# Optimization experiments

Measured on AMD Instinct MI355X. Metric: run time of the kernel, lower is better.

The kernel has to match this reference:

```python
import jax, jax.numpy as jnp
import numpy as np


def _conv3x3(x, w, b):
    # standard 3x3 conv, stride 1, padding 1, NCHW/OIHW
    y = jax.lax.conv_general_dilated(
        x, w, window_strides=(1, 1), padding=((1, 1), (1, 1)),
        dimension_numbers=('NCHW', 'OIHW', 'NCHW'))
    return y + b[None, :, None, None]


def _deform_conv3x3(x, offset, w, b):
    # torchvision-style DeformConv2d: kernel 3x3, stride 1, pad 1, dilation 1,
    # 1 offset group, no mask. offset: [B, 18, H, W] with (dy, dx) per tap.
    B, C, H, W = x.shape
    K = 9
    off = offset.reshape(B, K, 2, H, W)
    ky = (jnp.arange(K) // 3 - 1).astype(x.dtype)[None, :, None, None]
    kx = (jnp.arange(K) % 3 - 1).astype(x.dtype)[None, :, None, None]
    # fractional sample positions per output pixel and kernel tap: [B, K, H, W]
    sy = off[:, :, 0] + ky + jnp.arange(H, dtype=x.dtype)[None, None, :, None]
    sx = off[:, :, 1] + kx + jnp.arange(W, dtype=x.dtype)[None, None, None, :]
    y0f = jnp.floor(sy)
    x0f = jnp.floor(sx)
    dy = sy - y0f
    dx = sx - x0f
    y0 = y0f.astype(jnp.int32)
    x0 = x0f.astype(jnp.int32)

    def sample_b(xb, yi, xi):
        # xb: [C,H,W], yi/xi: [K,H,W] -> [C,K,H,W], zero outside bounds
        valid = (yi >= 0) & (yi < H) & (xi >= 0) & (xi < W)
        yc = jnp.clip(yi, 0, H - 1)
        xc = jnp.clip(xi, 0, W - 1)
        return xb[:, yc, xc] * valid[None].astype(xb.dtype)

    def bilinear_b(xb, y0b, x0b, dyb, dxb):
        v00 = sample_b(xb, y0b, x0b)
        v01 = sample_b(xb, y0b, x0b + 1)
        v10 = sample_b(xb, y0b + 1, x0b)
        v11 = sample_b(xb, y0b + 1, x0b + 1)
        w00 = ((1 - dyb) * (1 - dxb))[None]
        w01 = ((1 - dyb) * dxb)[None]
        w10 = (dyb * (1 - dxb))[None]
        w11 = (dyb * dxb)[None]
        return v00 * w00 + v01 * w01 + v10 * w10 + v11 * w11

    samp = jax.vmap(bilinear_b)(x, y0, x0, dy, dx)  # [B, C, K, H, W]
    Co, Ci = w.shape[0], w.shape[1]
    out = jnp.einsum('oik,bikhw->bohw', w.reshape(Co, Ci, K), samp)
    return out + b[None, :, None, None]


def setup_inputs() -> dict:
    key = jax.random.key(0)
    ks = jax.random.split(key, 5)
    B, C, H, W = 4, 128, 96, 96
    lr = jax.random.normal(ks[0], (B, C, H, W), jnp.float32)
    hr = jax.random.normal(ks[1], (B, C, H, W), jnp.float32)
    w_off = jax.random.normal(ks[2], (18, 2 * C, 3, 3), jnp.float32) * 0.02
    b_off = jnp.zeros((18,), jnp.float32)
    w_def = jax.random.normal(ks[3], (C, C, 3, 3), jnp.float32) / np.float32(np.sqrt(C * 9))
    b_def = jax.random.normal(ks[4], (C,), jnp.float32) * 0.01
    return {"lr_features": lr, "hr_features": hr, "w_off": w_off,
            "b_off": b_off, "w_def": w_def, "b_def": b_def}


def reference(lr_features, hr_features, w_off, b_off, w_def, b_def):
    inp = jnp.concatenate([lr_features, hr_features], axis=1)  # [B, 2C, H, W]
    offset = _conv3x3(inp, w_off, b_off)                        # [B, 18, H, W]
    return _deform_conv3x3(hr_features, offset, w_def, b_def)   # [B, C, H, W]
```

## Files before the change

### kernel.cpp

```cpp
#include <hip/hip_runtime.h>
#include <hip/hip_bf16.h>

#define HH 96
#define WW 96
#define CC 128
#define C2 256
#define PLANE (HH*WW)
#define NGRP 6
#define GP 8
#define NG 16
#define KSG 72
#define ROWS 13
#define NPCHK (ROWS*WW)
#define PCHK_PAD 1280

typedef __attribute__((ext_vector_type(8))) short bf16x8;
typedef __attribute__((ext_vector_type(4))) float f32x4;
typedef __attribute__((ext_vector_type(4))) unsigned int u32x4;

__device__ __forceinline__ int swz(int row, int byte_in_row) {
    return row * 128 + (byte_in_row ^ ((row & 7) << 4));
}

__device__ __forceinline__ void gload_lds16(const void* g, void* l) {
    __builtin_amdgcn_global_load_lds(
        (const __attribute__((address_space(1))) char*)g,
        (__attribute__((address_space(3))) char*)l, 16, 0, 0);
}

__device__ __forceinline__ unsigned pack2(float a, float b) {
    return (unsigned)__bfloat16_as_ushort(__float2bfloat16(a)) |
           ((unsigned)__bfloat16_as_ushort(__float2bfloat16(b)) << 16);
}

#define MFMA16(A,B,C) __builtin_amdgcn_mfma_f32_16x16x32_bf16((A),(B),(C),0,0,0)

#define VMW4() { asm volatile("s_waitcnt vmcnt(4)" ::: "memory"); __builtin_amdgcn_sched_barrier(0); }
#define VMW0() { asm volatile("s_waitcnt vmcnt(0)" ::: "memory"); __builtin_amdgcn_sched_barrier(0); }
#define LGKM0_BAR() { asm volatile("s_waitcnt lgkmcnt(0)" ::: "memory"); \
    __builtin_amdgcn_sched_barrier(0); __builtin_amdgcn_s_barrier(); \
    __builtin_amdgcn_sched_barrier(0); }
#define RAW_BAR() { __builtin_amdgcn_sched_barrier(0); __builtin_amdgcn_s_barrier(); \
    __builtin_amdgcn_sched_barrier(0); }

__global__ __launch_bounds__(256) void prep_kernel(
    const float* __restrict__ hr, const float* __restrict__ lr,
    const float* __restrict__ w_def, const float* __restrict__ w_off,
    unsigned short* __restrict__ hrbf, unsigned short* __restrict__ lrbf,
    unsigned short* __restrict__ wpad, unsigned short* __restrict__ wop)
{
    const int bid = blockIdx.x;
    const int tid = threadIdx.x;
    if (bid < 4608) {
        const bool is_hr = bid < 2304;
        const float* src0 = is_hr ? hr : lr;
        unsigned short* o = is_hr ? hrbf : lrbf;
        int idx = (is_hr ? bid : bid - 2304) * 256 + tid;
        int hw = idx % PLANE;
        int t  = idx / PLANE;
        int g  = t & 15;
        int b  = t >> 4;
        const float* src = src0 + ((size_t)(b * CC + g * GP)) * PLANE + hw;
        unsigned pk[4];
#pragma unroll
        for (int j = 0; j < 4; ++j)
            pk[j] = pack2(src[(size_t)(2*j) * PLANE], src[(size_t)(2*j+1) * PLANE]);
        u32x4 v = {pk[0], pk[1], pk[2], pk[3]};
        *reinterpret_cast<u32x4*>(o + (size_t)idx * 8) = v;
    } else if (bid < 5184) {
        int i = (bid - 4608) * 256 + tid;
        int oc = i / (NG * KSG);
        int r  = i - oc * (NG * KSG);
        int g  = r / KSG;
        int s  = r - g * KSG;
        int tap = s >> 3;
        int icoff = s & 7;
        wpad[i] = __bfloat16_as_ushort(__float2bfloat16(
            w_def[(size_t)(oc * CC + g * GP + icoff) * 9 + tap]));
    } else {
        int i = (bid - 5184) * 256 + tid;
        int oc = i / (32 * KSG);
        int r  = i - oc * (32 * KSG);
        int g  = r / KSG;
        int s  = r - g * KSG;
        int tap = s >> 3;
        int icoff = s & 7;
        int c = g * 8 + icoff;
        float v = (oc < 18) ? w_off[(size_t)(oc * C2 + c) * 9 + tap] : 0.f;
        wop[i] = __bfloat16_as_ushort(__float2bfloat16(v));
    }
}

__global__ __launch_bounds__(256) void wcvt_kernel(const float* __restrict__ w,
                                                   unsigned short* __restrict__ o)
{
    int i = blockIdx.x * 256 + threadIdx.x;
    if (i < CC * NG * KSG) {
        int oc = i / (NG * KSG);
        int r  = i - oc * (NG * KSG);
        int g  = r / KSG;
        int s  = r - g * KSG;
        int tap = s >> 3;
        int icoff = s & 7;
        o[i] = __bfloat16_as_ushort(__float2bfloat16(
            w[(size_t)(oc * CC + g * GP + icoff) * 9 + tap]));
    }
}

__global__ __launch_bounds__(256) void cvt8_kernel(const float* __restrict__ src0,
                                                   unsigned short* __restrict__ o)
{
    int idx = blockIdx.x * 256 + threadIdx.x;
    int hw = idx % PLANE;
    int t  = idx / PLANE;
    int g  = t & 15;
    int b  = t >> 4;
    const float* src = src0 + ((size_t)(b * CC + g * GP)) * PLANE + hw;
    unsigned pk[4];
#pragma unroll
    for (int j = 0; j < 4; ++j)
        pk[j] = pack2(src[(size_t)(2*j) * PLANE], src[(size_t)(2*j+1) * PLANE]);
    u32x4 v = {pk[0], pk[1], pk[2], pk[3]};
    *reinterpret_cast<u32x4*>(o + (size_t)idx * 8) = v;
}

__global__ __launch_bounds__(256) void offset_conv_kernel(
    const float* __restrict__ lr, const float* __restrict__ hr,
    const float* __restrict__ w_off, float* __restrict__ outp)
{
    __shared__ float tile[2][324];
    const int bid = blockIdx.x;
    const int q   = bid % NGRP;
    const int t   = bid / NGRP;
    const int b   = t / 36;
    const int rr  = t % 36;
    const int h0  = (rr / 6) * 16;
    const int w0  = (rr % 6) * 16;
    const int tid = threadIdx.x;
    const int py  = tid >> 4;
    const int px  = tid & 15;

    const int c0 = (C2 * q) / NGRP, c1 = (C2 * (q + 1)) / NGRP;
    const float* srcp = (q < 3) ? lr : hr;
    const int cofs = (q < 3) ? 0 : CC;

    int gy0 = h0 - 1 + tid / 18, gx0 = w0 - 1 + tid % 18;
    bool ok0 = (unsigned)gy0 < (unsigned)HH && (unsigned)gx0 < (unsigned)WW;
    int off0 = gy0 * WW + gx0;
    int j1 = tid + 256;
    int gy1 = h0 - 1 + j1 / 18, gx1 = w0 - 1 + j1 % 18;
    bool ok1 = (j1 < 324) && (unsigned)gy1 < (unsigned)HH && (unsigned)gx1 < (unsigned)WW;
    int off1 = gy1 * WW + gx1;

    float acc[18];
#pragma unroll
    for (int oc = 0; oc < 18; ++oc) acc[oc] = 0.f;

    const float* pl = srcp + (size_t)(b * CC + c0 - cofs) * PLANE;
    float p0 = ok0 ? pl[off0] : 0.f;
    float p1 = ok1 ? pl[off1] : 0.f;

    for (int c = c0; c < c1; ++c) {
        float* tb = tile[c & 1];
        tb[tid] = p0;
        if (j1 < 324) tb[j1] = p1;
        __syncthreads();
        if (c + 1 < c1) {
            const float* pn = srcp + (size_t)(b * CC + c + 1 - cofs) * PLANE;
            p0 = ok0 ? pn[off0] : 0.f;
            p1 = ok1 ? pn[off1] : 0.f;
        }
        float tv[9];
#pragma unroll
        for (int ky = 0; ky < 3; ++ky)
#pragma unroll
            for (int kx = 0; kx < 3; ++kx)
                tv[ky*3+kx] = tb[(py+ky)*18 + px + kx];
#pragma unroll
        for (int oc = 0; oc < 18; ++oc) {
            const float* wp = w_off + (size_t)(oc * C2 + c) * 9;
#pragma unroll
            for (int tap = 0; tap < 9; ++tap)
                acc[oc] = fmaf(wp[tap], tv[tap], acc[oc]);
        }
    }
#pragma unroll
    for (int oc = 0; oc < 18; ++oc)
        outp[((size_t)(b*CC + q*18 + oc)) * PLANE + (h0+py)*WW + (w0+px)] = acc[oc];
}

__global__ __launch_bounds__(768, 6) void offset_mfma_kernel(
    const unsigned short* __restrict__ lrbf, const unsigned short* __restrict__ hrbf,
    const unsigned short* __restrict__ wop, const float* __restrict__ b_off,
    float* __restrict__ offw)
{
    __shared__ __align__(16) unsigned short planes[2][2][3*WW*8];
    __shared__ __align__(16) unsigned short wgt0[2][32*64];
    __shared__ __align__(16) unsigned short wgt1[2][32*8];
    __shared__ __align__(16) unsigned short samp0[2][WW*64];
    __shared__ __align__(16) unsigned short samp1[2][WW*8];

    const int rawb = blockIdx.x;
    const int bid  = (rawb & 7) * 48 + (rawb >> 3);
    const int b    = bid / HH;
    const int h    = bid % HH;
    const int tid  = threadIdx.x;

    const int pri = tid / 96, ppx = tid - (tid / 96) * 96;
    const int prow = min(max(h - 1 + pri, 0), HH - 1);

    const int woc = tid / 9, wsl = tid % 9;
    float4 wv0, wv1;

#define ISSUE_P2(PAIR, PB) { \
    if (tid < 288) { \
        int gA_ = 2*(PAIR), gB_ = gA_ + 1; \
        const unsigned short* bA_ = (gA_ < 16 ? lrbf : hrbf); \
        const unsigned short* bB_ = (gB_ < 16 ? lrbf : hrbf); \
        gload_lds16(bA_ + ((size_t)(b*16 + (gA_ & 15)) * PLANE + prow*WW + ppx) * 8, \
                    (char*)planes[PB][0] + tid*16); \
        gload_lds16(bB_ + ((size_t)(b*16 + (gB_ & 15)) * PLANE + prow*WW + ppx) * 8, \
                    (char*)planes[PB][1] + tid*16); \
    } }
#define ISSUE_W2(PAIR) { \
    if (tid < 288) { \
        wv0 = *reinterpret_cast<const float4*>(wop + ((size_t)(woc*32 + 2*(PAIR)    ))*KSG + wsl*8); \
        wv1 = *reinterpret_cast<const float4*>(wop + ((size_t)(woc*32 + 2*(PAIR) + 1))*KSG + wsl*8); \
    } }
#define WRITE_W2() { \
    if (tid < 288) { \
        if (wsl < 8) { \
            *reinterpret_cast<float4*>((char*)wgt0[0] + swz(woc, wsl*16)) = wv0; \
            *reinterpret_cast<float4*>((char*)wgt0[1] + swz(woc, wsl*16)) = wv1; \
        } else { \
            *reinterpret_cast<float4*>((char*)wgt1[0] + woc*16) = wv0; \
            *reinterpret_cast<float4*>((char*)wgt1[1] + woc*16) = wv1; \
        } \
    } }

    const int tap1 = tid / WW, px1 = tid - (tid / WW) * WW;
    const int ky1 = tap1 / 3 - 1, kx1 = tap1 % 3 - 1;
    const int row1 = h + ky1, x1 = px1 + kx1;
    const bool ok1 = (unsigned)row1 < (unsigned)HH && (unsigned)x1 < (unsigned)WW;
    const int ro1 = ((ky1+1)*WW + x1) * 16;
    const int wr1 = px1*128 + ((tap1*16) ^ ((px1 & 7) << 4));
    const int x2 = tid + 1;
    const bool ok2 = (tid < 96) && (h + 1 < HH) && (x2 < WW);
    const int ro2 = (2*WW + x2) * 16;
    const int wr2 = tid * 16;

    const int lane = tid & 63;
    const int wid  = tid >> 6;
    const int ocg  = wid / 6;
    const int pxg  = wid - ocg * 6;
    const int l15  = lane & 15;
    const int l4   = lane >> 4;
    const int rowA = ocg*16 + l15;
    const int rowB = pxg*16 + l15;
    const bf16x8 zf = {};

    f32x4 acc = (f32x4){0.f, 0.f, 0.f, 0.f};

#define MFMA_O2() { \
    _Pragma("unroll") \
    for (int q_ = 0; q_ < 2; ++q_) { \
        bf16x8 a0_ = *reinterpret_cast<const bf16x8*>((char*)wgt0[q_] + swz(rowA, l4*16)); \
        bf16x8 a1_ = *reinterpret_cast<const bf16x8*>((char*)wgt0[q_] + swz(rowA, 64 + l4*16)); \
        bf16x8 a2_ = *reinterpret_cast<const bf16x8*>((char*)wgt1[q_] + rowA*16); \
        if (l4) a2_ = zf; \
        bf16x8 b0_ = *reinterpret_cast<const bf16x8*>((char*)samp0[q_] + swz(rowB, l4*16)); \
        bf16x8 b1_ = *reinterpret_cast<const bf16x8*>((char*)samp0[q_] + swz(rowB, 64 + l4*16)); \
        bf16x8 b2_ = *reinterpret_cast<const bf16x8*>((char*)samp1[q_] + rowB*16); \
        acc = MFMA16(a0_, b0_, acc); \
        acc = MFMA16(a1_, b1_, acc); \
        acc = MFMA16(a2_, b2_, acc); \
    } }

    ISSUE_W2(0);
    ISSUE_P2(0, 0);
    __syncthreads();

    for (int p2 = 0; p2 < 16; ++p2) {
        const int sb = p2 & 1;
        WRITE_W2();
        if (p2 < 15) {
            ISSUE_W2(p2 + 1);
            ISSUE_P2(p2 + 1, sb ^ 1);
            VMW4();
        } else {
            VMW0();
        }
        RAW_BAR();
        {
            u32x4 vA = {0u, 0u, 0u, 0u}, vB = {0u, 0u, 0u, 0u};
            if (ok1) {
                vA = *reinterpret_cast<const u32x4*>((const char*)planes[sb][0] + ro1);
                vB = *reinterpret_cast<const u32x4*>((const char*)planes[sb][1] + ro1);
            }
            *reinterpret_cast<u32x4*>((char*)samp0[0] + wr1) = vA;
            *reinterpret_cast<u32x4*>((char*)samp0[1] + wr1) = vB;
            if (tid < 96) {
                u32x4 wA = {0u, 0u, 0u, 0u}, wB = {0u, 0u, 0u, 0u};
                if (ok2) {
                    wA = *reinterpret_cast<const u32x4*>((const char*)planes[sb][0] + ro2);
                    wB = *reinterpret_cast<const u32x4*>((const char*)planes[sb][1] + ro2);
                }
                *reinterpret_cast<u32x4*>((char*)samp1[0] + wr2) = wA;
                *reinterpret_cast<u32x4*>((char*)samp1[1] + wr2) = wB;
            }
        }
        LGKM0_BAR();
        __builtin_amdgcn_s_setprio(1);
        MFMA_O2();
        __builtin_amdgcn_s_setprio(0);
        RAW_BAR();
    }

#pragma unroll
    for (int r = 0; r < 4; ++r) {
        int oc = ocg*16 + l4*4 + r;
        if (oc < 18)
            offw[((size_t)(b*18 + oc)) * PLANE + h*WW + pxg*16 + l15] = acc[r] + b_off[oc];
    }
#undef ISSUE_P2
#undef ISSUE_W2
#undef WRITE_W2
#undef MFMA_O2
}

template<bool HRBF, bool OFFWS>
__global__ __launch_bounds__(768, 6) void deform2_kernel(
    const float* __restrict__ hr, const unsigned short* __restrict__ hrbf,
    const float* __restrict__ b_off, const unsigned short* __restrict__ wpad,
    const float* __restrict__ b_def, const float* __restrict__ offw,
    float* __restrict__ outp)
{
    __shared__ __align__(16) unsigned short planes[2][PCHK_PAD*8];
    __shared__ __align__(16) unsigned short wgt0[CC*64];
    __shared__ __align__(16) unsigned short wgt1[CC*8];
    __shared__ __align__(16) unsigned short samp0[WW*64];
    __shared__ __align__(16) unsigned short samp1[WW*8];
    __shared__ __align__(8)  float2 geom[9*97];
    __shared__ float bias_lds[CC];

    const int rawb = blockIdx.x;
    const int bid  = (rawb & 7) * 48 + (rawb >> 3);
    const int b    = bid / HH;
    const int h    = bid % HH;
    const int tid  = threadIdx.x;
    const int r0   = min(max(h - 6, 0), HH - ROWS);

    const float* hrb = hr + (size_t)b * CC * PLANE;

    float4 wv0, wv1;
    const int wc0oc = tid / 9, wc0s = tid % 9;
    const int wt2   = (tid < 384) ? tid + 768 : tid;
    const int wc1oc = wt2 / 9, wc1s = wt2 % 9;
    const int pc2   = (tid < 512) ? tid + 768 : tid;
    const int pcs   = min(pc2, NPCHK - 1);

#define ISSUE_WGT(G) { \
    wv0 = *reinterpret_cast<const float4*>(wpad + ((size_t)(wc0oc*NG + (G))*KSG + wc0s*8)); \
    wv1 = *reinterpret_cast<const float4*>(wpad + ((size_t)(wc1oc*NG + (G))*KSG + wc1s*8)); }
#define WRITE_WGT() { \
    if (wc0s < 8) *reinterpret_cast<float4*>((char*)wgt0 + swz(wc0oc, wc0s*16)) = wv0; \
    else          *reinterpret_cast<float4*>((char*)wgt1 + wc0oc*16) = wv0; \
    if (tid < 384) { \
        if (wc1s < 8) *reinterpret_cast<float4*>((char*)wgt0 + swz(wc1oc, wc1s*16)) = wv1; \
        else          *reinterpret_cast<float4*>((char*)wgt1 + wc1oc*16) = wv1; \
    } }

#define ISSUE_PLANES(G, PB) { \
    const unsigned short* src_ = hrbf + ((size_t)(b*NG + (G))*PLANE + r0*WW)*8; \
    gload_lds16(src_ + (size_t)tid*8, (char*)planes[PB] + tid*16); \
    gload_lds16(src_ + (size_t)pcs*8, (char*)planes[PB] + pc2*16); }

#define STAGE_DIRECT(G, PB) { \
    for (int p = tid; p < NPCHK; p += 768) { \
        int r_ = p / WW, x_ = p - (p / WW) * WW; \
        const float* s_ = hrb + (size_t)((G)*GP) * PLANE + (r0 + r_)*WW + x_; \
        unsigned pk_[4]; \
        _Pragma("unroll") \
        for (int j = 0; j < 4; ++j) \
            pk_[j] = pack2(s_[(size_t)(2*j)*PLANE], s_[(size_t)(2*j+1)*PLANE]); \
        u32x4 v_ = {pk_[0], pk_[1], pk_[2], pk_[3]}; \
        *reinterpret_cast<u32x4*>((char*)planes[PB] + p*16) = v_; \
    } }

    if (HRBF) ISSUE_PLANES(0, 0);
    ISSUE_WGT(0);

    for (int t = tid; t < 9 * WW; t += 768) {
        int tap = t / WW;
        int px  = t - tap * WW;
        int hw  = h * WW + px;
        float offy, offx;
        if (OFFWS) {
            offy = offw[((size_t)(b*18 + 2*tap    )) * PLANE + hw];
            offx = offw[((size_t)(b*18 + 2*tap + 1)) * PLANE + hw];
        } else {
            offy = b_off[2*tap]; offx = b_off[2*tap + 1];
#pragma unroll
            for (int q = 0; q < NGRP; ++q) {
                offy += outp[((size_t)(b*CC + q*18 + 2*tap    )) * PLANE + hw];
                offx += outp[((size_t)(b*CC + q*18 + 2*tap + 1)) * PLANE + hw];
            }
        }
        geom[tap*97 + px] = make_float2((float)h  + (float)(tap/3 - 1) + offy,
                                        (float)px + (float)(tap%3 - 1) + offx);
    }
    if (tid < CC) bias_lds[tid] = b_def[tid];
    if (!HRBF) STAGE_DIRECT(0, 0);
    __syncthreads();

    const int lane = tid & 63;
    const int wid  = tid >> 6;
    const int ocg4 = wid / 3;
    const int pxg  = wid - ocg4 * 3;
    const int l15  = lane & 15;
    const int l4   = lane >> 4;

    f32x4 acc[2][2];
#pragma unroll
    for (int mf = 0; mf < 2; ++mf)
#pragma unroll
        for (int nf = 0; nf < 2; ++nf)
            acc[mf][nf] = (f32x4){0.f, 0.f, 0.f, 0.f};

    const int rowA0 = ocg4*32 + l15, rowA1 = rowA0 + 16;
    const int rowB0 = pxg*32 + l15,  rowB1 = rowB0 + 16;
    const bf16x8 zf = {};

#define MFMA_G() { \
    bf16x8 a00_ = *reinterpret_cast<const bf16x8*>((char*)wgt0 + swz(rowA0, l4*16)); \
    bf16x8 a10_ = *reinterpret_cast<const bf16x8*>((char*)wgt0 + swz(rowA1, l4*16)); \
    bf16x8 a01_ = *reinterpret_cast<const bf16x8*>((char*)wgt0 + swz(rowA0, 64 + l4*16)); \
    bf16x8 a11_ = *reinterpret_cast<const bf16x8*>((char*)wgt0 + swz(rowA1, 64 + l4*16)); \
    bf16x8 a02_ = *reinterpret_cast<const bf16x8*>((char*)wgt1 + rowA0*16); \
    bf16x8 a12_ = *reinterpret_cast<const bf16x8*>((char*)wgt1 + rowA1*16); \
    if (l4) { a02_ = zf; a12_ = zf; } \
    const char* s0_ = (const char*)samp0; \
    const char* s1_ = (const char*)samp1; \
    bf16x8 b00_ = *reinterpret_cast<const bf16x8*>(s0_ + swz(rowB0, l4*16)); \
    bf16x8 b10_ = *reinterpret_cast<const bf16x8*>(s0_ + swz(rowB1, l4*16)); \
    bf16x8 b01_ = *reinterpret_cast<const bf16x8*>(s0_ + swz(rowB0, 64 + l4*16)); \
    bf16x8 b11_ = *reinterpret_cast<const bf16x8*>(s0_ + swz(rowB1, 64 + l4*16)); \
    bf16x8 b02_ = *reinterpret_cast<const bf16x8*>(s1_ + rowB0*16); \
    bf16x8 b12_ = *reinterpret_cast<const bf16x8*>(s1_ + rowB1*16); \
    acc[0][0] = MFMA16(a00_, b00_, acc[0][0]); \
    acc[0][1] = MFMA16(a00_, b10_, acc[0][1]); \
    acc[1][0] = MFMA16(a10_, b00_, acc[1][0]); \
    acc[1][1] = MFMA16(a10_, b10_, acc[1][1]); \
    acc[0][0] = MFMA16(a01_, b01_, acc[0][0]); \
    acc[0][1] = MFMA16(a01_, b11_, acc[0][1]); \
    acc[1][0] = MFMA16(a11_, b01_, acc[1][0]); \
    acc[1][1] = MFMA16(a11_, b11_, acc[1][1]); \
    acc[0][0] = MFMA16(a02_, b02_, acc[0][0]); \
    acc[0][1] = MFMA16(a02_, b12_, acc[0][1]); \
    acc[1][0] = MFMA16(a12_, b02_, acc[1][0]); \
    acc[1][1] = MFMA16(a12_, b12_, acc[1][1]); }

    for (int g = 0; g < NG; ++g) {
        const int pb = g & 1;
        WRITE_WGT();
        if (g < NG - 1) {
            ISSUE_WGT(g + 1);
            if (HRBF) { ISSUE_PLANES(g + 1, pb ^ 1); }
            else      { STAGE_DIRECT(g + 1, pb ^ 1); }
            if (HRBF) { VMW4(); }
        } else {
            if (HRBF) { VMW0(); }
        }
        for (int it = tid; it < 9 * WW; it += 768) {
            int tap = it / WW;
            int px  = it - tap * WW;
            float2 s2 = geom[tap*97 + px];
            float sy = s2.x, sx = s2.y;
            float y0f = floorf(sy), x0f = floorf(sx);
            float dy = sy - y0f, dx = sx - x0f;
            int y0 = (int)y0f, x0 = (int)x0f;
            bool y0v = (unsigned)y0       < (unsigned)HH;
            bool y1v = (unsigned)(y0 + 1) < (unsigned)HH;
            bool x0v = (unsigned)x0       < (unsigned)WW;
            bool x1v = (unsigned)(x0 + 1) < (unsigned)WW;
            float ody = 1.f - dy, odx = 1.f - dx;
            float w00 = (y0v && x0v) ? ody*odx : 0.f;
            float w01 = (y0v && x1v) ? ody*dx  : 0.f;
            float w10 = (y1v && x0v) ? dy*odx  : 0.f;
            float w11 = (y1v && x1v) ? dy*dx   : 0.f;
            int y0c = min(max(y0, 0), HH-1), y1c = min(max(y0+1, 0), HH-1);
            int x0c = min(max(x0, 0), WW-1), x1c = min(max(x0+1, 0), WW-1);
            float sv[GP];
            bool ng = (y0v && (unsigned)(y0 - r0) >= (unsigned)ROWS) ||
                      (y1v && (unsigned)(y1c - r0) >= (unsigned)ROWS);
            if (__builtin_expect(!ng, 1)) {
                int ra = min(max(y0c - r0, 0), ROWS-1);
                int rb = min(max(y1c - r0, 0), ROWS-1);
                const char* pbase = (const char*)planes[pb];
                u32x4 q00 = *reinterpret_cast<const u32x4*>(pbase + (ra*WW + x0c)*16);
                u32x4 q01 = *reinterpret_cast<const u32x4*>(pbase + (ra*WW + x1c)*16);
                u32x4 q10 = *reinterpret_cast<const u32x4*>(pbase + (rb*WW + x0c)*16);
                u32x4 q11 = *reinterpret_cast<const u32x4*>(pbase + (rb*WW + x1c)*16);
#pragma unroll
                for (int j = 0; j < 4; ++j) {
                    float a00 = __uint_as_float(q00[j] << 16), b00 = __uint_as_float(q00[j] & 0xffff0000u);
                    float a01 = __uint_as_float(q01[j] << 16), b01 = __uint_as_float(q01[j] & 0xffff0000u);
                    float a10 = __uint_as_float(q10[j] << 16), b10 = __uint_as_float(q10[j] & 0xffff0000u);
                    float a11 = __uint_as_float(q11[j] << 16), b11 = __uint_as_float(q11[j] & 0xffff0000u);
                    sv[2*j]   = fmaf(w00, a00, fmaf(w01, a01, fmaf(w10, a10, w11*a11)));
                    sv[2*j+1] = fmaf(w00, b00, fmaf(w01, b01, fmaf(w10, b10, w11*b11)));
                }
            } else {
                const float* base = hrb + (size_t)(g*GP) * PLANE;
#pragma unroll
                for (int j = 0; j < GP; ++j) {
                    const float* p = base + (size_t)j * PLANE;
                    sv[j] = fmaf(w00, p[y0c*WW + x0c], fmaf(w01, p[y0c*WW + x1c],
                            fmaf(w10, p[y1c*WW + x0c], w11 * p[y1c*WW + x1c])));
                }
            }
            unsigned pk0 = pack2(sv[0], sv[1]), pk1 = pack2(sv[2], sv[3]);
            unsigned pk2 = pack2(sv[4], sv[5]), pk3 = pack2(sv[6], sv[7]);
            u32x4 pv = {pk0, pk1, pk2, pk3};
            if (tap < 8)
                *reinterpret_cast<u32x4*>((char*)samp0 + swz(px, tap*16)) = pv;
            else
                *reinterpret_cast<u32x4*>((char*)samp1 + px*16) = pv;
        }
        LGKM0_BAR();
        __builtin_amdgcn_s_setprio(1);
        MFMA_G();
        __builtin_amdgcn_s_setprio(0);
        RAW_BAR();
    }

#pragma unroll
    for (int mf = 0; mf < 2; ++mf)
#pragma unroll
        for (int r = 0; r < 4; ++r) {
            int oc = ocg4*32 + mf*16 + l4*4 + r;
            float bd = bias_lds[oc];
#pragma unroll
            for (int nf = 0; nf < 2; ++nf) {
                int px = pxg*32 + nf*16 + l15;
                outp[((size_t)(b*CC + oc)) * PLANE + h*WW + px] = acc[mf][nf][r] + bd;
            }
        }
#undef ISSUE_WGT
#undef WRITE_WGT
#undef ISSUE_PLANES
#undef STAGE_DIRECT
#undef MFMA_G
}

extern "C" void kernel_launch(void* const* d_in, const int* in_sizes, int n_in,
                              void* d_out, int out_size, void* d_ws, size_t ws_size,
                              hipStream_t stream)
{
    const float* lr    = (const float*)d_in[0];
    const float* hr    = (const float*)d_in[1];
    const float* w_off = (const float*)d_in[2];
    const float* b_off = (const float*)d_in[3];
    const float* w_def = (const float*)d_in[4];
    const float* b_def = (const float*)d_in[5];
    float* outp = (float*)d_out;

    const size_t wpad_b = (size_t)CC * NG * KSG * 2 + 256;
    const size_t hrbf_b = (size_t)4 * NG * PLANE * GP * 2;
    const size_t lrbf_b = hrbf_b;
    const size_t woff_b = (size_t)32 * 32 * KSG * 2 + 256;
    const size_t offw_b = (size_t)4 * 18 * PLANE * 4;

    unsigned short* wpad = (unsigned short*)d_ws;
    unsigned short* hrbf = (unsigned short*)((char*)d_ws + wpad_b);
    unsigned short* lrbf = (unsigned short*)((char*)d_ws + wpad_b + hrbf_b);
    unsigned short* wop  = (unsigned short*)((char*)d_ws + wpad_b + hrbf_b + lrbf_b);
    float*          offw = (float*)((char*)d_ws + wpad_b + hrbf_b + lrbf_b + woff_b);

    const bool full     = ws_size >= wpad_b + hrbf_b + lrbf_b + woff_b + offw_b;
    const bool use_hrbf = ws_size >= wpad_b + hrbf_b + lrbf_b;

    if (full) {
        prep_kernel<<<5472, 256, 0, stream>>>(hr, lr, w_def, w_off,
                                              hrbf, lrbf, wpad, wop);
        offset_mfma_kernel<<<4*HH, 768, 0, stream>>>(lrbf, hrbf, wop, b_off, offw);
        deform2_kernel<true, true><<<4*HH, 768, 0, stream>>>(
            hr, hrbf, b_off, wpad, b_def, offw, outp);
    } else {
        wcvt_kernel<<<(CC*NG*KSG + 255)/256, 256, 0, stream>>>(w_def, wpad);
        if (use_hrbf)
            cvt8_kernel<<<(4*NG*PLANE)/256, 256, 0, stream>>>(hr, hrbf);
        offset_conv_kernel<<<4*36*NGRP, 256, 0, stream>>>(lr, hr, w_off, outp);
        if (use_hrbf)
            deform2_kernel<true, false><<<4*HH, 768, 0, stream>>>(
                hr, hrbf, b_off, wpad, b_def, offw, outp);
        else
            deform2_kernel<false, false><<<4*HH, 768, 0, stream>>>(
                hr, hrbf, b_off, wpad, b_def, offw, outp);
    }
}
```

Measured before the change: 99.15 us.

## Replace staged-plane deform kernel with direct global bilinear gathers and precomputed geometry

Adds a new deform3 kernel that drops the LDS-staged input plane chunks and instead gathers the four bilinear corner vectors (8 bf16 channels each) straight from global memory. Per-pixel tap geometry (clamped indices and masked bilinear weights) is computed once per block into LDS and reused across all 16 channel groups. It also frees the large planes buffer in LDS. The cost is more global and L2 traffic from unstaged, partly redundant gathers, with less control over latency hiding.

Result: faster. 91.54 us (-7.7%).

```diff
diff --git a/kernel.cpp b/kernel.cpp
--- a/kernel.cpp
+++ b/kernel.cpp
@@ -326,6 +326,180 @@
 #undef ISSUE_W2
 #undef WRITE_W2
 #undef MFMA_O2
+}
+
+__global__ __launch_bounds__(768, 6) void deform3_kernel(
+    const unsigned short* __restrict__ hrbf, const unsigned short* __restrict__ wpad,
+    const float* __restrict__ b_def, const float* __restrict__ offw,
+    float* __restrict__ outp)
+{
+    __shared__ __align__(16) unsigned short wgt0[CC*64];
+    __shared__ __align__(16) unsigned short wgt1[CC*8];
+    __shared__ __align__(16) unsigned short samp0[WW*64];
+    __shared__ __align__(16) unsigned short samp1[WW*8];
+    __shared__ __align__(16) float4 gw4[9*WW];
+    __shared__ __align__(8)  short4 gyo[9*WW];
+    __shared__ float bias_lds[CC];
+
+    const int rawb = blockIdx.x;
+    const int bid  = (rawb & 7) * 48 + (rawb >> 3);
+    const int b    = bid / HH;
+    const int h    = bid % HH;
+    const int tid  = threadIdx.x;
+
+    float4 wv0, wv1;
+    const int wc0oc = tid / 9, wc0s = tid % 9;
+    const int wt2   = (tid < 384) ? tid + 768 : tid;
+    const int wc1oc = wt2 / 9, wc1s = wt2 % 9;
+
+#define ISSUE_WGT(G) { \
+    wv0 = *reinterpret_cast<const float4*>(wpad + ((size_t)(wc0oc*NG + (G))*KSG + wc0s*8)); \
+    wv1 = *reinterpret_cast<const float4*>(wpad + ((size_t)(wc1oc*NG + (G))*KSG + wc1s*8)); }
+#define WRITE_WGT() { \
+    if (wc0s < 8) *reinterpret_cast<float4*>((char*)wgt0 + swz(wc0oc, wc0s*16)) = wv0; \
+    else          *reinterpret_cast<float4*>((char*)wgt1 + wc0oc*16) = wv0; \
+    if (tid < 384) { \
+        if (wc1s < 8) *reinterpret_cast<float4*>((char*)wgt0 + swz(wc1oc, wc1s*16)) = wv1; \
+        else          *reinterpret_cast<float4*>((char*)wgt1 + wc1oc*16) = wv1; \
+    } }
+
+    ISSUE_WGT(0);
+
+    for (int it = tid; it < 9 * WW; it += 768) {
+        int tap = it / WW;
+        int px  = it - tap * WW;
+        int hw  = h * WW + px;
+        float offy = offw[((size_t)(b*18 + 2*tap    )) * PLANE + hw];
+        float offx = offw[((size_t)(b*18 + 2*tap + 1)) * PLANE + hw];
+        float sy = (float)h  + (float)(tap/3 - 1) + offy;
+        float sx = (float)px + (float)(tap%3 - 1) + offx;
+        float y0f = floorf(sy), x0f = floorf(sx);
+        float dy = sy - y0f, dx = sx - x0f;
+        int y0 = (int)y0f, x0 = (int)x0f;
+        bool y0v = (unsigned)y0       < (unsigned)HH;
+        bool y1v = (unsigned)(y0 + 1) < (unsigned)HH;
+        bool x0v = (unsigned)x0       < (unsigned)WW;
+        bool x1v = (unsigned)(x0 + 1) < (unsigned)WW;
+        float ody = 1.f - dy, odx = 1.f - dx;
+        float4 wv;
+        wv.x = (y0v && x0v) ? ody*odx : 0.f;
+        wv.y = (y0v && x1v) ? ody*dx  : 0.f;
+        wv.z = (y1v && x0v) ? dy*odx  : 0.f;
+        wv.w = (y1v && x1v) ? dy*dx   : 0.f;
+        short4 o4;
+        o4.x = (short)min(max(y0,     0), HH-1);
+        o4.y = (short)min(max(y0 + 1, 0), HH-1);
+        o4.z = (short)min(max(x0,     0), WW-1);
+        o4.w = (short)min(max(x0 + 1, 0), WW-1);
+        gw4[it] = wv;
+        gyo[it] = o4;
+    }
+    if (tid < CC) bias_lds[tid] = b_def[tid];
+    __syncthreads();
+
+    const int lane = tid & 63;
+    const int wid  = tid >> 6;
+    const int ocg4 = wid / 3;
+    const int pxg  = wid - ocg4 * 3;
+    const int l15  = lane & 15;
+    const int l4   = lane >> 4;
+
+    f32x4 acc[2][2];
+#pragma unroll
+    for (int mf = 0; mf < 2; ++mf)
+#pragma unroll
+        for (int nf = 0; nf < 2; ++nf)
+            acc[mf][nf] = (f32x4){0.f, 0.f, 0.f, 0.f};
+
+    const int rowA0 = ocg4*32 + l15, rowA1 = rowA0 + 16;
+    const int rowB0 = pxg*32 + l15,  rowB1 = rowB0 + 16;
+    const bf16x8 zf = {};
+
+#define MFMA_G() { \
+    bf16x8 a00_ = *reinterpret_cast<const bf16x8*>((char*)wgt0 + swz(rowA0, l4*16)); \
+    bf16x8 a10_ = *reinterpret_cast<const bf16x8*>((char*)wgt0 + swz(rowA1, l4*16)); \
+    bf16x8 a01_ = *reinterpret_cast<const bf16x8*>((char*)wgt0 + swz(rowA0, 64 + l4*16)); \
+    bf16x8 a11_ = *reinterpret_cast<const bf16x8*>((char*)wgt0 + swz(rowA1, 64 + l4*16)); \
+    bf16x8 a02_ = *reinterpret_cast<const bf16x8*>((char*)wgt1 + rowA0*16); \
+    bf16x8 a12_ = *reinterpret_cast<const bf16x8*>((char*)wgt1 + rowA1*16); \
+    if (l4) { a02_ = zf; a12_ = zf; } \
+    const char* s0_ = (const char*)samp0; \
+    const char* s1_ = (const char*)samp1; \
+    bf16x8 b00_ = *reinterpret_cast<const bf16x8*>(s0_ + swz(rowB0, l4*16)); \
+    bf16x8 b10_ = *reinterpret_cast<const bf16x8*>(s0_ + swz(rowB1, l4*16)); \
+    bf16x8 b01_ = *reinterpret_cast<const bf16x8*>(s0_ + swz(rowB0, 64 + l4*16)); \
+    bf16x8 b11_ = *reinterpret_cast<const bf16x8*>(s0_ + swz(rowB1, 64 + l4*16)); \
+    bf16x8 b02_ = *reinterpret_cast<const bf16x8*>(s1_ + rowB0*16); \
+    bf16x8 b12_ = *reinterpret_cast<const bf16x8*>(s1_ + rowB1*16); \
+    acc[0][0] = MFMA16(a00_, b00_, acc[0][0]); \
+    acc[0][1] = MFMA16(a00_, b10_, acc[0][1]); \
+    acc[1][0] = MFMA16(a10_, b00_, acc[1][0]); \
+    acc[1][1] = MFMA16(a10_, b10_, acc[1][1]); \
+    acc[0][0] = MFMA16(a01_, b01_, acc[0][0]); \
+    acc[0][1] = MFMA16(a01_, b11_, acc[0][1]); \
+    acc[1][0] = MFMA16(a11_, b01_, acc[1][0]); \
+    acc[1][1] = MFMA16(a11_, b11_, acc[1][1]); \
+    acc[0][0] = MFMA16(a02_, b02_, acc[0][0]); \
+    acc[0][1] = MFMA16(a02_, b12_, acc[0][1]); \
+    acc[1][0] = MFMA16(a12_, b02_, acc[1][0]); \
+    acc[1][1] = MFMA16(a12_, b12_, acc[1][1]); }
+
+    const unsigned short* gb = hrbf + (size_t)(b * NG) * PLANE * 8;
+
+    for (int g = 0; g < NG; ++g) {
+        WRITE_WGT();
+        if (g < NG - 1) ISSUE_WGT(g + 1);
+        const unsigned short* gpl = gb + (size_t)g * PLANE * 8;
+        for (int it = tid; it < 9 * WW; it += 768) {
+            float4 w4 = gw4[it];
+            short4 o4 = gyo[it];
+            int ra = (int)o4.x * WW, rb = (int)o4.y * WW;
+            u32x4 q00 = *reinterpret_cast<const u32x4*>(gpl + (size_t)(ra + o4.z) * 8);
+            u32x4 q01 = *reinterpret_cast<const u32x4*>(gpl + (size_t)(ra + o4.w) * 8);
+            u32x4 q10 = *reinterpret_cast<const u32x4*>(gpl + (size_t)(rb + o4.z) * 8);
+            u32x4 q11 = *reinterpret_cast<const u32x4*>(gpl + (size_t)(rb + o4.w) * 8);
+            float sv[GP];
+#pragma unroll
+            for (int j = 0; j < 4; ++j) {
+                float a00 = __uint_as_float(q00[j] << 16), b00 = __uint_as_float(q00[j] & 0xffff0000u);
+                float a01 = __uint_as_float(q01[j] << 16), b01 = __uint_as_float(q01[j] & 0xffff0000u);
+                float a10 = __uint_as_float(q10[j] << 16), b10 = __uint_as_float(q10[j] & 0xffff0000u);
+                float a11 = __uint_as_float(q11[j] << 16), b11 = __uint_as_float(q11[j] & 0xffff0000u);
+                sv[2*j]   = fmaf(w4.x, a00, fmaf(w4.y, a01, fmaf(w4.z, a10, w4.w*a11)));
+                sv[2*j+1] = fmaf(w4.x, b00, fmaf(w4.y, b01, fmaf(w4.z, b10, w4.w*b11)));
+            }
+            unsigned pk0 = pack2(sv[0], sv[1]), pk1 = pack2(sv[2], sv[3]);
+            unsigned pk2 = pack2(sv[4], sv[5]), pk3 = pack2(sv[6], sv[7]);
+            u32x4 pv = {pk0, pk1, pk2, pk3};
+            int tap = it / WW;
+            int px  = it - tap * WW;
+            if (tap < 8)
+                *reinterpret_cast<u32x4*>((char*)samp0 + swz(px, tap*16)) = pv;
+            else
+                *reinterpret_cast<u32x4*>((char*)samp1 + px*16) = pv;
+        }
+        LGKM0_BAR();
+        __builtin_amdgcn_s_setprio(1);
+        MFMA_G();
+        __builtin_amdgcn_s_setprio(0);
+        RAW_BAR();
+    }
+
+#pragma unroll
+    for (int mf = 0; mf < 2; ++mf)
+#pragma unroll
+        for (int r = 0; r < 4; ++r) {
+            int oc = ocg4*32 + mf*16 + l4*4 + r;
+            float bd = bias_lds[oc];
+#pragma unroll
+            for (int nf = 0; nf < 2; ++nf) {
+                int px = pxg*32 + nf*16 + l15;
+                outp[((size_t)(b*CC + oc)) * PLANE + h*WW + px] = acc[mf][nf][r] + bd;
+            }
+        }
+#undef ISSUE_WGT
+#undef WRITE_WGT
+#undef MFMA_G
 }
 
 template<bool HRBF, bool OFFWS>
@@ -584,8 +758,7 @@
         prep_kernel<<<5472, 256, 0, stream>>>(hr, lr, w_def, w_off,
                                               hrbf, lrbf, wpad, wop);
         offset_mfma_kernel<<<4*HH, 768, 0, stream>>>(lrbf, hrbf, wop, b_off, offw);
-        deform2_kernel<true, true><<<4*HH, 768, 0, stream>>>(
-            hr, hrbf, b_off, wpad, b_def, offw, outp);
+        deform3_kernel<<<4*HH, 768, 0, stream>>>(hrbf, wpad, b_def, offw, outp);
     } else {
         wcvt_kernel<<<(CC*NG*KSG + 255)/256, 256, 0, stream>>>(w_def, wpad);
         if (use_hrbf)
```
